# Performance work log

Hardware: AMD Instinct MI355X
Metric: run time of the kernel (lower is better)

Reference implementation:

```python
import jax, jax.numpy as jnp
import numpy as np

N_TOKENS = 4096
N_EMBD = 1024
N_EXPERTS = 8
TOP_K = 2
TEMPERATURE = 1.0
PARAM_SCALE = 0.02


def setup_inputs() -> dict:
    key = jax.random.key(0)
    ks = jax.random.split(key, 6)
    x = jax.random.normal(ks[0], (N_TOKENS, N_EMBD), dtype=jnp.float32)
    gate_w = jax.random.normal(ks[1], (N_EMBD, N_EXPERTS), dtype=jnp.float32) * PARAM_SCALE
    w1 = jax.random.normal(ks[2], (N_EXPERTS, N_EMBD, 4 * N_EMBD), dtype=jnp.float32) * PARAM_SCALE
    b1 = jax.random.normal(ks[3], (N_EXPERTS, 4 * N_EMBD), dtype=jnp.float32) * PARAM_SCALE
    w2 = jax.random.normal(ks[4], (N_EXPERTS, 4 * N_EMBD, N_EMBD), dtype=jnp.float32) * PARAM_SCALE
    b2 = jax.random.normal(ks[5], (N_EXPERTS, N_EMBD), dtype=jnp.float32) * PARAM_SCALE
    return {"x": x, "gate_w": gate_w, "w1": w1, "b1": b1, "w2": w2, "b2": b2}


def reference(x, gate_w, w1, b1, w2, b2):
    # Gating: softmax with temperature, top-2, renormalize over the top-2.
    gate_logits = x @ gate_w                              # [N, E]
    gate_probs = jax.nn.softmax(gate_logits / TEMPERATURE, axis=-1)
    top_v, top_i = jax.lax.top_k(gate_probs, TOP_K)       # [N, k]
    top_v = top_v / jnp.sum(top_v, axis=-1, keepdims=True)
    # Per-expert combine weight: sum of renormalized top-k probs routed to e.
    one_hot = jax.nn.one_hot(top_i, N_EXPERTS, dtype=x.dtype)   # [N, k, E]
    combine = jnp.einsum('nk,nke->ne', top_v, one_hot)          # [N, E]
    # Dense expert evaluation (faithful math; loop over fixed small expert set).
    out = jnp.zeros_like(x)
    for e in range(N_EXPERTS):
        h = jax.nn.gelu(x @ w1[e] + b1[e], approximate=False)   # [N, 4C]
        y = h @ w2[e] + b2[e]                                   # [N, C]
        out = out + combine[:, e:e + 1] * y
    return out
```

## Files before the change

### kernel.cpp

```cpp
#include <hip/hip_runtime.h>
#include <math.h>

#define TOKENS 4096
#define EMBD   1024
#define HID    4096
#define NE     8
#define SLOTC  8320

typedef __attribute__((ext_vector_type(8))) short short8;
typedef __attribute__((ext_vector_type(4))) float f32x4;

#define GLOBAL_PTR(p) ((const __attribute__((address_space(1))) void*)(p))
#define LDS_PTR(p)    ((__attribute__((address_space(3))) void*)(p))

#define SWZ(row, q) ((row) * 32 + (((q) ^ (((row) >> 1) & 3)) * 8))

__device__ __forceinline__ unsigned short f2bf(float f) {
  unsigned int u = __float_as_uint(f);
  u += 0x7FFFu + ((u >> 16) & 1u);
  return (unsigned short)(u >> 16);
}
__device__ __forceinline__ float bf2f(unsigned short h) {
  return __uint_as_float((unsigned int)h << 16);
}

__device__ __forceinline__ float fast_gelu(float v) {
  float u = fabsf(v) * 0.70710678118654752f;
  float t = 1.0f / (1.0f + 0.3275911f * u);
  float poly = ((((1.061405429f * t - 1.453152027f) * t + 1.421413741f) * t
                 - 0.284496736f) * t + 0.254829592f) * t;
  float erf_abs = 1.0f - poly * __expf(-u * u);
  float er = (v < 0.0f) ? -erf_abs : erf_abs;
  return 0.5f * v * (1.0f + er);
}

__global__ void k_zero_ctrl(int* __restrict__ ctrl) {
  if (threadIdx.x < 32) ctrl[threadIdx.x] = 0;
}

__global__ __launch_bounds__(256) void k_gate_cvt(const float* __restrict__ x,
                                                  const float* __restrict__ gw,
                                                  unsigned short* __restrict__ xb,
                                                  int* __restrict__ idx2,
                                                  float* __restrict__ wv,
                                                  int* __restrict__ ctrl) {
  int wave = threadIdx.x >> 6, lane = threadIdx.x & 63;
  int t = blockIdx.x * 4 + wave;
  const float4* xr = (const float4*)(x + (size_t)t * EMBD);
  ushort4* xbr = (ushort4*)(xb + (size_t)t * EMBD);
  float acc[NE];
#pragma unroll
  for (int e = 0; e < NE; e++) acc[e] = 0.f;
#pragma unroll
  for (int ch = 0; ch < 4; ch++) {
    int i = ch * 64 + lane;
    float4 v = xr[i];
    ushort4 o;
    o.x = f2bf(v.x); o.y = f2bf(v.y); o.z = f2bf(v.z); o.w = f2bf(v.w);
    xbr[i] = o;
    int c = i * 4;
    const float* g0 = gw + (size_t)c * NE;
#pragma unroll
    for (int e = 0; e < NE; e++) acc[e] += v.x * g0[e];
#pragma unroll
    for (int e = 0; e < NE; e++) acc[e] += v.y * g0[NE + e];
#pragma unroll
    for (int e = 0; e < NE; e++) acc[e] += v.z * g0[2 * NE + e];
#pragma unroll
    for (int e = 0; e < NE; e++) acc[e] += v.w * g0[3 * NE + e];
  }
#pragma unroll
  for (int e = 0; e < NE; e++) {
#pragma unroll
    for (int off = 32; off > 0; off >>= 1) acc[e] += __shfl_down(acc[e], off);
  }
  if (lane == 0) {
    float best = -1e30f, second = -1e30f;
    int bi = 0, si = 0;
#pragma unroll
    for (int e = 0; e < NE; e++) {
      float l = acc[e];
      if (l > best) { second = best; si = bi; best = l; bi = e; }
      else if (l > second) { second = l; si = e; }
    }
    float b = expf(second - best);
    float w0 = 1.f / (1.f + b);
    float w1 = b / (1.f + b);
    idx2[2 * t] = bi; idx2[2 * t + 1] = si;
    wv[2 * t] = w0; wv[2 * t + 1] = w1;
    atomicAdd(&ctrl[bi], 1);
    atomicAdd(&ctrl[si], 1);
  }
}

__global__ void k_scan(int* __restrict__ ctrl) {
  if (threadIdx.x == 0) {
    int off = 0;
    for (int e = 0; e < NE; e++) { ctrl[8 + e] = off; off += ctrl[e]; }
    ctrl[16] = off;
  }
  if (threadIdx.x < NE) ctrl[17 + threadIdx.x] = 0;
}

__global__ __launch_bounds__(256) void k_assign(const int* __restrict__ idx2,
                                                const float* __restrict__ wv,
                                                int* __restrict__ ctrl,
                                                int* __restrict__ token_list,
                                                float* __restrict__ slot_w,
                                                int* __restrict__ tok2slot) {
  int t = blockIdx.x * 256 + threadIdx.x;
  if (t >= TOKENS) return;
#pragma unroll
  for (int k = 0; k < 2; k++) {
    int e = idx2[2 * t + k];
    int pos = atomicAdd(&ctrl[17 + e], 1);
    int slot = ctrl[8 + e] + pos;
    token_list[slot] = t;
    slot_w[slot] = wv[2 * t + k];
    tok2slot[2 * t + k] = slot;
  }
}

__global__ __launch_bounds__(256) void k_trans(const float* __restrict__ in,
                                               unsigned short* __restrict__ out,
                                               int R, int C) {
  __shared__ unsigned short T[64 * 66];
  int e = blockIdx.z;
  const float* ine = in + (size_t)e * R * C;
  unsigned short* oute = out + (size_t)e * R * C;
  int r0 = blockIdx.y * 64;
  int c0 = blockIdx.x * 64;
  int tid = threadIdx.x;
  {
    int c4 = tid & 15;
    int rb = tid >> 4;
#pragma unroll
    for (int it = 0; it < 4; it++) {
      int r = rb + 16 * it;
      float4 v = *(const float4*)(ine + (size_t)(r0 + r) * C + c0 + 4 * c4);
      T[(4 * c4 + 0) * 66 + r] = f2bf(v.x);
      T[(4 * c4 + 1) * 66 + r] = f2bf(v.y);
      T[(4 * c4 + 2) * 66 + r] = f2bf(v.z);
      T[(4 * c4 + 3) * 66 + r] = f2bf(v.w);
    }
  }
  __syncthreads();
  {
    int rr = tid & 7;
    int cq = tid >> 3;
#pragma unroll
    for (int it = 0; it < 2; it++) {
      int c = cq + 32 * it;
      short8 o;
#pragma unroll
      for (int k = 0; k < 8; k++) o[k] = (short)T[c * 66 + 8 * rr + k];
      *(short8*)(oute + (size_t)(c0 + c) * R + r0 + 8 * rr) = o;
    }
  }
}

__global__ __launch_bounds__(256, 2) void k_gemm1(
    const unsigned short* __restrict__ xb,
    const unsigned short* __restrict__ w1t,
    const float* __restrict__ b1,
    const int* __restrict__ ctrl,
    const int* __restrict__ token_list,
    unsigned short* __restrict__ Hbuf) {
  int h = blockIdx.x;
  int e = h & 7;
  int j = h >> 3;
  int nb = (j & 31) * 128;
  int m_base = (j >> 5) * 128;
  int cnt = ctrl[e];
  if (m_base >= cnt) return;
  int off_e = ctrl[8 + e];
  int tid = threadIdx.x;
  int wave = tid >> 6, lane = tid & 63;

  __shared__ __align__(16) unsigned short As[128 * 32];
  __shared__ __align__(16) unsigned short Bs[128 * 32];

  int chS = (tid & 3) ^ ((tid >> 3) & 3);
  int rowA0 = tid >> 2;
  int rowA1 = 64 + (tid >> 2);
  int tok0 = token_list[off_e + min(m_base + rowA0, cnt - 1)];
  int tok1 = token_list[off_e + min(m_base + rowA1, cnt - 1)];
  const unsigned short* srcA0 = xb + (size_t)tok0 * EMBD + chS * 8;
  const unsigned short* srcA1 = xb + (size_t)tok1 * EMBD + chS * 8;
  const unsigned short* wb = w1t + (size_t)e * HID * EMBD;
  const unsigned short* srcB0 = wb + (size_t)(nb + rowA0) * EMBD + chS * 8;
  const unsigned short* srcB1 = wb + (size_t)(nb + rowA1) * EMBD + chS * 8;
  char* AsB = (char*)As;
  char* BsB = (char*)Bs;

  f32x4 acc[4][4];
#pragma unroll
  for (int i = 0; i < 4; i++)
#pragma unroll
    for (int j2 = 0; j2 < 4; j2++) acc[i][j2] = (f32x4){0.f, 0.f, 0.f, 0.f};

  int wm = (wave >> 1) * 64, wn = (wave & 1) * 64;
  int q4 = lane >> 4, cc = lane & 15;

  for (int k0 = 0; k0 < EMBD; k0 += 32) {
    __builtin_amdgcn_global_load_lds(GLOBAL_PTR(srcA0 + k0), LDS_PTR(AsB + wave * 1024), 16, 0, 0);
    __builtin_amdgcn_global_load_lds(GLOBAL_PTR(srcA1 + k0), LDS_PTR(AsB + 4096 + wave * 1024), 16, 0, 0);
    __builtin_amdgcn_global_load_lds(GLOBAL_PTR(srcB0 + k0), LDS_PTR(BsB + wave * 1024), 16, 0, 0);
    __builtin_amdgcn_global_load_lds(GLOBAL_PTR(srcB1 + k0), LDS_PTR(BsB + 4096 + wave * 1024), 16, 0, 0);
    __syncthreads();
    short8 af[4], bfr[4];
#pragma unroll
    for (int i = 0; i < 4; i++)
      af[i] = *(const short8*)(As + SWZ(wm + i * 16 + cc, q4));
#pragma unroll
    for (int j2 = 0; j2 < 4; j2++)
      bfr[j2] = *(const short8*)(Bs + SWZ(wn + j2 * 16 + cc, q4));
#pragma unroll
    for (int i = 0; i < 4; i++)
#pragma unroll
      for (int j2 = 0; j2 < 4; j2++)
        acc[i][j2] = __builtin_amdgcn_mfma_f32_16x16x32_bf16(af[i], bfr[j2], acc[i][j2], 0, 0, 0);
    __syncthreads();
  }

  const float* b1e = b1 + (size_t)e * HID;
  float bias[4];
#pragma unroll
  for (int j2 = 0; j2 < 4; j2++) bias[j2] = b1e[nb + wn + j2 * 16 + cc];
#pragma unroll
  for (int i = 0; i < 4; i++) {
#pragma unroll
    for (int r = 0; r < 4; r++) {
      int m_loc = wm + i * 16 + q4 * 4 + r;
      int m = m_base + m_loc;
      if (m < cnt) {
        size_t hrow = (size_t)(off_e + m) * HID;
#pragma unroll
        for (int j2 = 0; j2 < 4; j2++)
          Hbuf[hrow + nb + wn + j2 * 16 + cc] = f2bf(fast_gelu(acc[i][j2][r] + bias[j2]));
      }
    }
  }
}

__global__ __launch_bounds__(256, 2) void k_gemm2(
    const unsigned short* __restrict__ Hbuf,
    const unsigned short* __restrict__ w2t,
    const int* __restrict__ ctrl,
    unsigned short* __restrict__ Yp) {
  int h = blockIdx.x;
  int e = h & 7;
  int s = (h >> 3) & 1;
  int rem = h >> 4;
  int m_base = (rem >> 3) * 128;
  int nb = (rem & 7) * 128;
  int cnt = ctrl[e];
  if (m_base >= cnt) return;
  int off_e = ctrl[8 + e];
  int tid = threadIdx.x;
  int wave = tid >> 6, lane = tid & 63;

  __shared__ __align__(16) unsigned short As[128 * 32];
  __shared__ __align__(16) unsigned short Bs[128 * 32];

  int chS = (tid & 3) ^ ((tid >> 3) & 3);
  int rowA0 = tid >> 2;
  int rowA1 = 64 + (tid >> 2);
  const unsigned short* srcA0 = Hbuf + (size_t)(off_e + m_base + rowA0) * HID + chS * 8;
  const unsigned short* srcA1 = Hbuf + (size_t)(off_e + m_base + rowA1) * HID + chS * 8;
  const unsigned short* wb = w2t + (size_t)e * EMBD * HID;
  const unsigned short* srcB0 = wb + (size_t)(nb + rowA0) * HID + chS * 8;
  const unsigned short* srcB1 = wb + (size_t)(nb + rowA1) * HID + chS * 8;
  char* AsB = (char*)As;
  char* BsB = (char*)Bs;

  f32x4 acc[4][4];
#pragma unroll
  for (int i = 0; i < 4; i++)
#pragma unroll
    for (int j2 = 0; j2 < 4; j2++) acc[i][j2] = (f32x4){0.f, 0.f, 0.f, 0.f};

  int wm = (wave >> 1) * 64, wn = (wave & 1) * 64;
  int q4 = lane >> 4, cc = lane & 15;

  int kbeg = s * (HID / 2), kend = kbeg + HID / 2;
  for (int k0 = kbeg; k0 < kend; k0 += 32) {
    __builtin_amdgcn_global_load_lds(GLOBAL_PTR(srcA0 + k0), LDS_PTR(AsB + wave * 1024), 16, 0, 0);
    __builtin_amdgcn_global_load_lds(GLOBAL_PTR(srcA1 + k0), LDS_PTR(AsB + 4096 + wave * 1024), 16, 0, 0);
    __builtin_amdgcn_global_load_lds(GLOBAL_PTR(srcB0 + k0), LDS_PTR(BsB + wave * 1024), 16, 0, 0);
    __builtin_amdgcn_global_load_lds(GLOBAL_PTR(srcB1 + k0), LDS_PTR(BsB + 4096 + wave * 1024), 16, 0, 0);
    __syncthreads();
    short8 af[4], bfr[4];
#pragma unroll
    for (int i = 0; i < 4; i++)
      af[i] = *(const short8*)(As + SWZ(wm + i * 16 + cc, q4));
#pragma unroll
    for (int j2 = 0; j2 < 4; j2++)
      bfr[j2] = *(const short8*)(Bs + SWZ(wn + j2 * 16 + cc, q4));
#pragma unroll
    for (int i = 0; i < 4; i++)
#pragma unroll
      for (int j2 = 0; j2 < 4; j2++)
        acc[i][j2] = __builtin_amdgcn_mfma_f32_16x16x32_bf16(af[i], bfr[j2], acc[i][j2], 0, 0, 0);
    __syncthreads();
  }

  unsigned short* Yps = Yp + (size_t)s * SLOTC * EMBD;
#pragma unroll
  for (int i = 0; i < 4; i++) {
#pragma unroll
    for (int r = 0; r < 4; r++) {
      int m_loc = wm + i * 16 + q4 * 4 + r;
      int m = m_base + m_loc;
      if (m < cnt) {
        size_t yrow = (size_t)(off_e + m) * EMBD;
#pragma unroll
        for (int j2 = 0; j2 < 4; j2++)
          Yps[yrow + nb + wn + j2 * 16 + cc] = f2bf(acc[i][j2][r]);
      }
    }
  }
}

__global__ __launch_bounds__(256) void k_combine(const unsigned short* __restrict__ Yp,
                                                 const float* __restrict__ b2,
                                                 const int* __restrict__ idx2,
                                                 const float* __restrict__ wv,
                                                 const int* __restrict__ tok2slot,
                                                 float* __restrict__ out) {
  int t = blockIdx.x;
  int tid = threadIdx.x;
  int c = tid * 4;
  int e0 = idx2[2 * t], e1 = idx2[2 * t + 1];
  float w0 = wv[2 * t], w1 = wv[2 * t + 1];
  int s0 = tok2slot[2 * t], s1 = tok2slot[2 * t + 1];
  ushort4 p00 = *(const ushort4*)(Yp + ((size_t)0 * SLOTC + s0) * EMBD + c);
  ushort4 p01 = *(const ushort4*)(Yp + ((size_t)1 * SLOTC + s0) * EMBD + c);
  ushort4 p10 = *(const ushort4*)(Yp + ((size_t)0 * SLOTC + s1) * EMBD + c);
  ushort4 p11 = *(const ushort4*)(Yp + ((size_t)1 * SLOTC + s1) * EMBD + c);
  float4 b20 = *(const float4*)(b2 + (size_t)e0 * EMBD + c);
  float4 b21 = *(const float4*)(b2 + (size_t)e1 * EMBD + c);
  float4 r;
  r.x = w0 * (bf2f(p00.x) + bf2f(p01.x) + b20.x) + w1 * (bf2f(p10.x) + bf2f(p11.x) + b21.x);
  r.y = w0 * (bf2f(p00.y) + bf2f(p01.y) + b20.y) + w1 * (bf2f(p10.y) + bf2f(p11.y) + b21.y);
  r.z = w0 * (bf2f(p00.z) + bf2f(p01.z) + b20.z) + w1 * (bf2f(p10.z) + bf2f(p11.z) + b21.z);
  r.w = w0 * (bf2f(p00.w) + bf2f(p01.w) + b20.w) + w1 * (bf2f(p10.w) + bf2f(p11.w) + b21.w);
  *(float4*)(out + (size_t)t * EMBD + c) = r;
}

extern "C" void kernel_launch(void* const* d_in, const int* in_sizes, int n_in,
                              void* d_out, int out_size, void* d_ws, size_t ws_size,
                              hipStream_t stream) {
  (void)in_sizes; (void)n_in; (void)out_size; (void)ws_size;
  const float* x      = (const float*)d_in[0];
  const float* gate_w = (const float*)d_in[1];
  const float* w1     = (const float*)d_in[2];
  const float* b1     = (const float*)d_in[3];
  const float* w2     = (const float*)d_in[4];
  const float* b2     = (const float*)d_in[5];
  float* out = (float*)d_out;

  char* ws = (char*)d_ws;
  size_t off = 0;
  auto alloc = [&](size_t bytes) {
    char* p = ws + off;
    off += (bytes + 255) & ~(size_t)255;
    return p;
  };
  unsigned short* xb    = (unsigned short*)alloc((size_t)TOKENS * EMBD * 2);
  unsigned short* w1t   = (unsigned short*)alloc((size_t)NE * HID * EMBD * 2);
  unsigned short* w2t   = (unsigned short*)alloc((size_t)NE * EMBD * HID * 2);
  unsigned short* Hbuf  = (unsigned short*)alloc((size_t)SLOTC * HID * 2);
  unsigned short* Yp    = (unsigned short*)alloc((size_t)2 * SLOTC * EMBD * 2);
  int*   token_list     = (int*)alloc((size_t)SLOTC * 4);
  float* slot_w         = (float*)alloc((size_t)SLOTC * 4);
  int*   idx2           = (int*)alloc((size_t)TOKENS * 2 * 4);
  float* wv             = (float*)alloc((size_t)TOKENS * 2 * 4);
  int*   tok2slot       = (int*)alloc((size_t)TOKENS * 2 * 4);
  int*   ctrl           = (int*)alloc(32 * 4);

  k_zero_ctrl<<<1, 64, 0, stream>>>(ctrl);
  k_gate_cvt<<<TOKENS / 4, 256, 0, stream>>>(x, gate_w, xb, idx2, wv, ctrl);
  k_scan<<<1, 64, 0, stream>>>(ctrl);
  k_assign<<<TOKENS / 256, 256, 0, stream>>>(idx2, wv, ctrl, token_list, slot_w, tok2slot);
  k_trans<<<dim3(HID / 64, EMBD / 64, NE), 256, 0, stream>>>(w1, w1t, EMBD, HID);
  k_trans<<<dim3(EMBD / 64, HID / 64, NE), 256, 0, stream>>>(w2, w2t, HID, EMBD);
  k_gemm1<<<8192, 256, 0, stream>>>(xb, w1t, b1, ctrl, token_list, Hbuf);
  k_gemm2<<<4096, 256, 0, stream>>>(Hbuf, w2t, ctrl, Yp);
  k_combine<<<TOKENS, 256, 0, stream>>>(Yp, b2, idx2, wv, tok2slot, out);
}
```

Before: 691.6 us.

## Double-buffer LDS tiles in expert GEMMs and streamline routing count/assign

Both expert GEMM kernels now use two LDS buffers, so the next K-slice is issued via global_load_lds before MFMAs run on the current slice, removing one barrier per iteration and overlapping load latency with compute. Routing is also reworked: global atomics in the gate kernel plus the separate zero and scan kernels are replaced by a single-block shared-memory histogram/scan kernel, and assignment uses block-local atomics with one global atomic per expert per block. Doubling LDS per block may reduce occupancy, and slot order within an expert now depends on block atomics.

Result: faster. 561.4 us (-18.8%).

```diff
diff --git a/kernel.cpp b/kernel.cpp
--- a/kernel.cpp
+++ b/kernel.cpp
@@ -34,16 +34,11 @@
   return 0.5f * v * (1.0f + er);
 }
 
-__global__ void k_zero_ctrl(int* __restrict__ ctrl) {
-  if (threadIdx.x < 32) ctrl[threadIdx.x] = 0;
-}
-
 __global__ __launch_bounds__(256) void k_gate_cvt(const float* __restrict__ x,
                                                   const float* __restrict__ gw,
                                                   unsigned short* __restrict__ xb,
                                                   int* __restrict__ idx2,
-                                                  float* __restrict__ wv,
-                                                  int* __restrict__ ctrl) {
+                                                  float* __restrict__ wv) {
   int wave = threadIdx.x >> 6, lane = threadIdx.x & 63;
   int t = blockIdx.x * 4 + wave;
   const float4* xr = (const float4*)(x + (size_t)t * EMBD);
@@ -88,37 +83,48 @@
     float w1 = b / (1.f + b);
     idx2[2 * t] = bi; idx2[2 * t + 1] = si;
     wv[2 * t] = w0; wv[2 * t + 1] = w1;
-    atomicAdd(&ctrl[bi], 1);
-    atomicAdd(&ctrl[si], 1);
-  }
-}
-
-__global__ void k_scan(int* __restrict__ ctrl) {
-  if (threadIdx.x == 0) {
+  }
+}
+
+__global__ __launch_bounds__(256) void k_count(const int* __restrict__ idx2,
+                                               int* __restrict__ ctrl) {
+  __shared__ int cnt[NE];
+  int tid = threadIdx.x;
+  if (tid < NE) cnt[tid] = 0;
+  __syncthreads();
+  for (int i = tid; i < TOKENS * 2; i += 256) atomicAdd(&cnt[idx2[i]], 1);
+  __syncthreads();
+  if (tid == 0) {
     int off = 0;
-    for (int e = 0; e < NE; e++) { ctrl[8 + e] = off; off += ctrl[e]; }
+#pragma unroll
+    for (int e = 0; e < NE; e++) { int c = cnt[e]; ctrl[e] = c; ctrl[8 + e] = off; off += c; }
     ctrl[16] = off;
   }
-  if (threadIdx.x < NE) ctrl[17 + threadIdx.x] = 0;
+  if (tid < NE) ctrl[17 + tid] = 0;
 }
 
 __global__ __launch_bounds__(256) void k_assign(const int* __restrict__ idx2,
-                                                const float* __restrict__ wv,
                                                 int* __restrict__ ctrl,
                                                 int* __restrict__ token_list,
-                                                float* __restrict__ slot_w,
                                                 int* __restrict__ tok2slot) {
-  int t = blockIdx.x * 256 + threadIdx.x;
-  if (t >= TOKENS) return;
-#pragma unroll
-  for (int k = 0; k < 2; k++) {
-    int e = idx2[2 * t + k];
-    int pos = atomicAdd(&ctrl[17 + e], 1);
-    int slot = ctrl[8 + e] + pos;
-    token_list[slot] = t;
-    slot_w[slot] = wv[2 * t + k];
-    tok2slot[2 * t + k] = slot;
-  }
+  __shared__ int lpos[NE];
+  __shared__ int lbase[NE];
+  int tid = threadIdx.x;
+  int t = blockIdx.x * 256 + tid;
+  if (tid < NE) lpos[tid] = 0;
+  __syncthreads();
+  int e0 = idx2[2 * t], e1 = idx2[2 * t + 1];
+  int p0 = atomicAdd(&lpos[e0], 1);
+  int p1 = atomicAdd(&lpos[e1], 1);
+  __syncthreads();
+  if (tid < NE) lbase[tid] = atomicAdd(&ctrl[17 + tid], lpos[tid]);
+  __syncthreads();
+  int s0 = ctrl[8 + e0] + lbase[e0] + p0;
+  int s1 = ctrl[8 + e1] + lbase[e1] + p1;
+  token_list[s0] = t;
+  token_list[s1] = t;
+  tok2slot[2 * t] = s0;
+  tok2slot[2 * t + 1] = s1;
 }
 
 __global__ __launch_bounds__(256) void k_trans(const float* __restrict__ in,
@@ -177,8 +183,8 @@
   int tid = threadIdx.x;
   int wave = tid >> 6, lane = tid & 63;
 
-  __shared__ __align__(16) unsigned short As[128 * 32];
-  __shared__ __align__(16) unsigned short Bs[128 * 32];
+  __shared__ __align__(16) unsigned short As[2][128 * 32];
+  __shared__ __align__(16) unsigned short Bs[2][128 * 32];
 
   int chS = (tid & 3) ^ ((tid >> 3) & 3);
   int rowA0 = tid >> 2;
@@ -190,8 +196,6 @@
   const unsigned short* wb = w1t + (size_t)e * HID * EMBD;
   const unsigned short* srcB0 = wb + (size_t)(nb + rowA0) * EMBD + chS * 8;
   const unsigned short* srcB1 = wb + (size_t)(nb + rowA1) * EMBD + chS * 8;
-  char* AsB = (char*)As;
-  char* BsB = (char*)Bs;
 
   f32x4 acc[4][4];
 #pragma unroll
@@ -202,26 +206,37 @@
   int wm = (wave >> 1) * 64, wn = (wave & 1) * 64;
   int q4 = lane >> 4, cc = lane & 15;
 
-  for (int k0 = 0; k0 < EMBD; k0 += 32) {
-    __builtin_amdgcn_global_load_lds(GLOBAL_PTR(srcA0 + k0), LDS_PTR(AsB + wave * 1024), 16, 0, 0);
-    __builtin_amdgcn_global_load_lds(GLOBAL_PTR(srcA1 + k0), LDS_PTR(AsB + 4096 + wave * 1024), 16, 0, 0);
-    __builtin_amdgcn_global_load_lds(GLOBAL_PTR(srcB0 + k0), LDS_PTR(BsB + wave * 1024), 16, 0, 0);
-    __builtin_amdgcn_global_load_lds(GLOBAL_PTR(srcB1 + k0), LDS_PTR(BsB + 4096 + wave * 1024), 16, 0, 0);
+#define STAGE1(buf, k0) do {                                                                            \
+    __builtin_amdgcn_global_load_lds(GLOBAL_PTR(srcA0 + (k0)), LDS_PTR((char*)&As[buf][0] + wave * 1024), 16, 0, 0);        \
+    __builtin_amdgcn_global_load_lds(GLOBAL_PTR(srcA1 + (k0)), LDS_PTR((char*)&As[buf][0] + 4096 + wave * 1024), 16, 0, 0); \
+    __builtin_amdgcn_global_load_lds(GLOBAL_PTR(srcB0 + (k0)), LDS_PTR((char*)&Bs[buf][0] + wave * 1024), 16, 0, 0);        \
+    __builtin_amdgcn_global_load_lds(GLOBAL_PTR(srcB1 + (k0)), LDS_PTR((char*)&Bs[buf][0] + 4096 + wave * 1024), 16, 0, 0); \
+  } while (0)
+
+#define COMPUTE1(buf) do {                                                                   \
+    short8 af[4], bfr[4];                                                                    \
+    _Pragma("unroll")                                                                        \
+    for (int i = 0; i < 4; i++) af[i] = *(const short8*)(&As[buf][0] + SWZ(wm + i * 16 + cc, q4));   \
+    _Pragma("unroll")                                                                        \
+    for (int j2 = 0; j2 < 4; j2++) bfr[j2] = *(const short8*)(&Bs[buf][0] + SWZ(wn + j2 * 16 + cc, q4)); \
+    _Pragma("unroll")                                                                        \
+    for (int i = 0; i < 4; i++)                                                              \
+      _Pragma("unroll")                                                                      \
+      for (int j2 = 0; j2 < 4; j2++)                                                         \
+        acc[i][j2] = __builtin_amdgcn_mfma_f32_16x16x32_bf16(af[i], bfr[j2], acc[i][j2], 0, 0, 0); \
+  } while (0)
+
+  STAGE1(0, 0);
+  __syncthreads();
+  int cur = 0;
+  for (int k0 = 32; k0 < EMBD; k0 += 32) {
+    STAGE1(cur ^ 1, k0);
+    __builtin_amdgcn_sched_barrier(0);
+    COMPUTE1(cur);
     __syncthreads();
-    short8 af[4], bfr[4];
-#pragma unroll
-    for (int i = 0; i < 4; i++)
-      af[i] = *(const short8*)(As + SWZ(wm + i * 16 + cc, q4));
-#pragma unroll
-    for (int j2 = 0; j2 < 4; j2++)
-      bfr[j2] = *(const short8*)(Bs + SWZ(wn + j2 * 16 + cc, q4));
-#pragma unroll
-    for (int i = 0; i < 4; i++)
-#pragma unroll
-      for (int j2 = 0; j2 < 4; j2++)
-        acc[i][j2] = __builtin_amdgcn_mfma_f32_16x16x32_bf16(af[i], bfr[j2], acc[i][j2], 0, 0, 0);
-    __syncthreads();
-  }
+    cur ^= 1;
+  }
+  COMPUTE1(cur);
 
   const float* b1e = b1 + (size_t)e * HID;
   float bias[4];
@@ -241,6 +256,8 @@
       }
     }
   }
+#undef STAGE1
+#undef COMPUTE1
 }
 
 __global__ __launch_bounds__(256, 2) void k_gemm2(
@@ -260,8 +277,8 @@
   int tid = threadIdx.x;
   int wave = tid >> 6, lane = tid & 63;
 
-  __shared__ __align__(16) unsigned short As[128 * 32];
-  __shared__ __align__(16) unsigned short Bs[128 * 32];
+  __shared__ __align__(16) unsigned short As[2][128 * 32];
+  __shared__ __align__(16) unsigned short Bs[2][128 * 32];
 
   int chS = (tid & 3) ^ ((tid >> 3) & 3);
   int rowA0 = tid >> 2;
@@ -271,8 +288,6 @@
   const unsigned short* wb = w2t + (size_t)e * EMBD * HID;
   const unsigned short* srcB0 = wb + (size_t)(nb + rowA0) * HID + chS * 8;
   const unsigned short* srcB1 = wb + (size_t)(nb + rowA1) * HID + chS * 8;
-  char* AsB = (char*)As;
-  char* BsB = (char*)Bs;
 
   f32x4 acc[4][4];
 #pragma unroll
@@ -283,27 +298,38 @@
   int wm = (wave >> 1) * 64, wn = (wave & 1) * 64;
   int q4 = lane >> 4, cc = lane & 15;
 
+#define STAGE2(buf, k0) do {                                                                            \
+    __builtin_amdgcn_global_load_lds(GLOBAL_PTR(srcA0 + (k0)), LDS_PTR((char*)&As[buf][0] + wave * 1024), 16, 0, 0);        \
+    __builtin_amdgcn_global_load_lds(GLOBAL_PTR(srcA1 + (k0)), LDS_PTR((char*)&As[buf][0] + 4096 + wave * 1024), 16, 0, 0); \
+    __builtin_amdgcn_global_load_lds(GLOBAL_PTR(srcB0 + (k0)), LDS_PTR((char*)&Bs[buf][0] + wave * 1024), 16, 0, 0);        \
+    __builtin_amdgcn_global_load_lds(GLOBAL_PTR(srcB1 + (k0)), LDS_PTR((char*)&Bs[buf][0] + 4096 + wave * 1024), 16, 0, 0); \
+  } while (0)
+
+#define COMPUTE2(buf) do {                                                                   \
+    short8 af[4], bfr[4];                                                                    \
+    _Pragma("unroll")                                                                        \
+    for (int i = 0; i < 4; i++) af[i] = *(const short8*)(&As[buf][0] + SWZ(wm + i * 16 + cc, q4));   \
+    _Pragma("unroll")                                                                        \
+    for (int j2 = 0; j2 < 4; j2++) bfr[j2] = *(const short8*)(&Bs[buf][0] + SWZ(wn + j2 * 16 + cc, q4)); \
+    _Pragma("unroll")                                                                        \
+    for (int i = 0; i < 4; i++)                                                              \
+      _Pragma("unroll")                                                                      \
+      for (int j2 = 0; j2 < 4; j2++)                                                         \
+        acc[i][j2] = __builtin_amdgcn_mfma_f32_16x16x32_bf16(af[i], bfr[j2], acc[i][j2], 0, 0, 0); \
+  } while (0)
+
   int kbeg = s * (HID / 2), kend = kbeg + HID / 2;
-  for (int k0 = kbeg; k0 < kend; k0 += 32) {
-    __builtin_amdgcn_global_load_lds(GLOBAL_PTR(srcA0 + k0), LDS_PTR(AsB + wave * 1024), 16, 0, 0);
-    __builtin_amdgcn_global_load_lds(GLOBAL_PTR(srcA1 + k0), LDS_PTR(AsB + 4096 + wave * 1024), 16, 0, 0);
-    __builtin_amdgcn_global_load_lds(GLOBAL_PTR(srcB0 + k0), LDS_PTR(BsB + wave * 1024), 16, 0, 0);
-    __builtin_amdgcn_global_load_lds(GLOBAL_PTR(srcB1 + k0), LDS_PTR(BsB + 4096 + wave * 1024), 16, 0, 0);
+  STAGE2(0, kbeg);
+  __syncthreads();
+  int cur = 0;
+  for (int k0 = kbeg + 32; k0 < kend; k0 += 32) {
+    STAGE2(cur ^ 1, k0);
+    __builtin_amdgcn_sched_barrier(0);
+    COMPUTE2(cur);
     __syncthreads();
-    short8 af[4], bfr[4];
-#pragma unroll
-    for (int i = 0; i < 4; i++)
-      af[i] = *(const short8*)(As + SWZ(wm + i * 16 + cc, q4));
-#pragma unroll
-    for (int j2 = 0; j2 < 4; j2++)
-      bfr[j2] = *(const short8*)(Bs + SWZ(wn + j2 * 16 + cc, q4));
-#pragma unroll
-    for (int i = 0; i < 4; i++)
-#pragma unroll
-      for (int j2 = 0; j2 < 4; j2++)
-        acc[i][j2] = __builtin_amdgcn_mfma_f32_16x16x32_bf16(af[i], bfr[j2], acc[i][j2], 0, 0, 0);
-    __syncthreads();
-  }
+    cur ^= 1;
+  }
+  COMPUTE2(cur);
 
   unsigned short* Yps = Yp + (size_t)s * SLOTC * EMBD;
 #pragma unroll
@@ -320,6 +346,8 @@
       }
     }
   }
+#undef STAGE2
+#undef COMPUTE2
 }
 
 __global__ __launch_bounds__(256) void k_combine(const unsigned short* __restrict__ Yp,
@@ -373,16 +401,14 @@
   unsigned short* Hbuf  = (unsigned short*)alloc((size_t)SLOTC * HID * 2);
   unsigned short* Yp    = (unsigned short*)alloc((size_t)2 * SLOTC * EMBD * 2);
   int*   token_list     = (int*)alloc((size_t)SLOTC * 4);
-  float* slot_w         = (float*)alloc((size_t)SLOTC * 4);
   int*   idx2           = (int*)alloc((size_t)TOKENS * 2 * 4);
   float* wv             = (float*)alloc((size_t)TOKENS * 2 * 4);
   int*   tok2slot       = (int*)alloc((size_t)TOKENS * 2 * 4);
   int*   ctrl           = (int*)alloc(32 * 4);
 
-  k_zero_ctrl<<<1, 64, 0, stream>>>(ctrl);
-  k_gate_cvt<<<TOKENS / 4, 256, 0, stream>>>(x, gate_w, xb, idx2, wv, ctrl);
-  k_scan<<<1, 64, 0, stream>>>(ctrl);
-  k_assign<<<TOKENS / 256, 256, 0, stream>>>(idx2, wv, ctrl, token_list, slot_w, tok2slot);
+  k_gate_cvt<<<TOKENS / 4, 256, 0, stream>>>(x, gate_w, xb, idx2, wv);
+  k_count<<<1, 256, 0, stream>>>(idx2, ctrl);
+  k_assign<<<TOKENS / 256, 256, 0, stream>>>(idx2, ctrl, token_list, tok2slot);
   k_trans<<<dim3(HID / 64, EMBD / 64, NE), 256, 0, stream>>>(w1, w1t, EMBD, HID);
   k_trans<<<dim3(EMBD / 64, HID / 64, NE), 256, 0, stream>>>(w2, w2t, HID, EMBD);
   k_gemm1<<<8192, 256, 0, stream>>>(xb, w1t, b1, ctrl, token_list, Hbuf);
```
